# Performance work log

Hardware: AMD Instinct MI355X
Metric: run time of the kernel (lower is better)

Reference implementation:

```python
import jax, jax.numpy as jnp
import numpy as np

ALPHA_FOCAL = 0.25
GAMMA_FOCAL = 2.0
MARGIN_PEN = 0.005
RADIUS_REP = 0.015


def _cdist(a, b):
    # a: [B,N,3], b: [B,M,3] -> [B,N,M] euclidean distances (torch.cdist)
    d2 = (jnp.sum(a * a, axis=-1)[:, :, None]
          + jnp.sum(b * b, axis=-1)[:, None, :]
          - 2.0 * jnp.einsum('bnd,bmd->bnm', a, b))
    return jnp.sqrt(jnp.maximum(d2, 1e-12))


def _chamfer(p1, p2):
    d = _cdist(p1, p2)                       # [B,N,M]
    return jnp.min(d, axis=2).mean(axis=1) + jnp.min(d, axis=1).mean(axis=1)


def _repulsion(pc):
    B, N, _ = pc.shape
    d = _cdist(pc, pc)
    d = jnp.where(jnp.eye(N, dtype=bool)[None], jnp.inf, d)
    return jax.nn.relu(RADIUS_REP - d).mean(axis=(1, 2))


def _penetration(hand_pc, obj_pc):
    d = _cdist(obj_pc, hand_pc)              # [B,Nobj,Nhand]
    min_d = jnp.min(d, axis=2)
    return jax.nn.relu(MARGIN_PEN - min_d).mean(axis=1)


def _focal(logits, y):
    # numerically-stable BCE with logits, reduction='none'
    bce = jnp.maximum(logits, 0.0) - logits * y + jnp.log1p(jnp.exp(-jnp.abs(logits)))
    pt = jnp.exp(-bce)
    return (ALPHA_FOCAL * (1.0 - pt) ** GAMMA_FOCAL * bce).mean()


def _pose_loss(pred_pose, gt_pose):
    loss_trans = jnp.abs(pred_pose[:, :3] - gt_pose[:, :3]).mean(axis=1)
    qp = pred_pose[:, 3:]
    qg = gt_pose[:, 3:]
    qp = qp / jnp.linalg.norm(qp, axis=1, keepdims=True)
    qg = qg / jnp.linalg.norm(qg, axis=1, keepdims=True)
    loss_rot = 1.0 - jnp.abs(jnp.sum(qp * qg, axis=1))
    return loss_trans + 0.1 * loss_rot


def setup_inputs() -> dict:
    key = jax.random.key(0)
    ks = jax.random.split(key, 11)
    B, NH, NO, DQ = 16, 1024, 2048, 24
    scale = 0.05  # meter-scale clouds so margins 0.005/0.015 are active
    return {
        'pred_hand': jax.random.normal(ks[0], (B, NH, 3)) * scale,
        'pred_obj': jax.random.normal(ks[1], (B, NO, 3)) * scale,
        'pred_pose': jax.random.normal(ks[2], (B, 7)),
        'pred_qpos': jax.random.normal(ks[3], (B, DQ)),
        'pred_contact_logits': jax.random.normal(ks[4], (B, NH)),
        'gt_hand': jax.random.normal(ks[5], (B, NH, 3)) * scale,
        'gt_obj': jax.random.normal(ks[6], (B, NO, 3)) * scale,
        'gt_pose': jax.random.normal(ks[7], (B, 7)),
        'gt_qpos': jax.random.normal(ks[8], (B, DQ)),
        'gt_contact': (jax.random.uniform(ks[9], (B, NH)) < 0.3).astype(jnp.float32),
        'has_contact': (jax.random.uniform(ks[10], (B,)) < 0.8).astype(jnp.float32),
    }


def reference(pred_hand, pred_obj, pred_pose, pred_qpos, pred_contact_logits,
              gt_hand, gt_obj, gt_pose, gt_qpos, gt_contact, has_contact):
    loss_cd_hand = _chamfer(pred_hand, gt_hand).mean()
    loss_qpos = jnp.mean((pred_qpos - gt_qpos) ** 2)
    loss_contact = _focal(pred_contact_logits, gt_contact)

    batch_cd_obj = _chamfer(pred_obj, gt_obj)
    batch_pose = _pose_loss(pred_pose, gt_pose)
    batch_rep = _repulsion(pred_obj)
    batch_pen = _penetration(pred_hand, pred_obj)

    valid = has_contact.sum() + 1e-6
    loss_cd_obj = jnp.sum(batch_cd_obj * has_contact) / valid
    loss_pose = jnp.sum(batch_pose * has_contact) / valid
    loss_rep = jnp.sum(batch_rep * has_contact) / valid
    loss_pen = jnp.sum(batch_pen * has_contact) / valid

    total = (5.0 * loss_cd_hand + 5.0 * loss_cd_obj + 2.0 * loss_pose
             + 1.0 * loss_qpos + 2.0 * loss_contact
             + 0.5 * loss_rep + 0.5 * loss_pen)
    return total
```

## Files before the change

### kernel.cpp

```cpp
#include <hip/hip_runtime.h>
#include <math.h>

#define B   16
#define NH  1024
#define NO  2048
#define DQ  24

#define ALPHA_FOCAL 0.25f
#define MARGIN_PEN  0.005f
#define RADIUS_REP  0.015f
#define R2REP       (RADIUS_REP * RADIUS_REP)

#define WS_SCAL    16
#define ROWS_TOTAL 131072
#define JC         128

typedef float v2f __attribute__((ext_vector_type(2)));
typedef float v4f __attribute__((ext_vector_type(4)));

__device__ inline float wsqrt(float x) { return __builtin_amdgcn_sqrtf(x); }

__device__ inline float block_reduce_sum(float v, float* red) {
    #pragma unroll
    for (int off = 32; off > 0; off >>= 1) v += __shfl_down(v, off, 64);
    int lane = threadIdx.x & 63;
    int wid  = threadIdx.x >> 6;
    if (lane == 0) red[wid] = v;
    __syncthreads();
    float s = 0.f;
    if (threadIdx.x == 0) s = red[0] + red[1] + red[2] + red[3];
    __syncthreads();
    return s;
}

__device__ inline void cham_step(v4f A, v4f Bv,
                                 const v2f px2[4], const v2f py2[4], const v2f pz2[4],
                                 v2f m2[4]) {
    v2f ax = A.lo, ay = A.hi, az = Bv.lo, aw = Bv.hi;
    #pragma unroll
    for (int k = 0; k < 4; ++k) {
        v2f t = __builtin_elementwise_fma(az, pz2[k], aw);
        t     = __builtin_elementwise_fma(ay, py2[k], t);
        t     = __builtin_elementwise_fma(ax, px2[k], t);
        m2[k] = __builtin_elementwise_min(m2[k], t);
    }
}

__device__ inline void rep_step(v4f A, v4f Bv,
                                const v2f px2[4], const v2f py2[4], const v2f pz2[4],
                                const v2f pn2[4], v2f* s2) {
    v2f ax = A.lo, ay = A.hi, az = Bv.lo, aw = Bv.hi;
    #pragma unroll
    for (int k = 0; k < 4; ++k) {
        v2f t = __builtin_elementwise_fma(az, pz2[k], aw);
        t     = __builtin_elementwise_fma(ay, py2[k], t);
        t     = __builtin_elementwise_fma(ax, px2[k], t);
        v2f d2 = t + pn2[k];
        v2f dd;
        dd.x = wsqrt(__builtin_amdgcn_fmed3f(d2.x, 1e-12f, R2REP));
        dd.y = wsqrt(__builtin_amdgcn_fmed3f(d2.y, 1e-12f, R2REP));
        *s2 += dd;
    }
}

__global__ __launch_bounds__(256, 4) void pairwise_kernel(
    const float* __restrict__ pred_hand, const float* __restrict__ pred_obj,
    const float* __restrict__ gt_hand,   const float* __restrict__ gt_obj,
    const float* __restrict__ has_contact,
    const float* __restrict__ logits,    const float* __restrict__ gt_contact,
    const float* __restrict__ pred_qpos, const float* __restrict__ gt_qpos,
    const float* __restrict__ pred_pose, const float* __restrict__ gt_pose,
    float* __restrict__ ws)
{
    __shared__ v4f  qs[JC];
    __shared__ float red[4];

    const int tid = threadIdx.x;
    const int blk = blockIdx.x;

    if (blk >= 2048) {
        if (blk == 2048) {
            float fsum = 0.f;
            for (int i = tid; i < B*NH; i += 256) {
                float l = logits[i];
                float y = gt_contact[i];
                float bce = fmaxf(l, 0.f) - l*y + log1pf(expf(-fabsf(l)));
                float pt  = expf(-bce);
                float om  = 1.f - pt;
                fsum += ALPHA_FOCAL * om * om * bce;
            }
            float fT = block_reduce_sum(fsum, red);
            if (tid == 0) atomicAdd(&ws[6], fT);
        } else if (blk == 2049) {
            float qsum = 0.f;
            for (int i = tid; i < B*DQ; i += 256) {
                float d = pred_qpos[i] - gt_qpos[i];
                qsum += d*d;
            }
            float qT = block_reduce_sum(qsum, red);
            if (tid == 0) atomicAdd(&ws[7], qT);
        } else {
            float psum = 0.f, vsum = 0.f;
            if (tid < B) {
                const float* pp = pred_pose + tid*7;
                const float* gp = gt_pose   + tid*7;
                float lt = (fabsf(pp[0]-gp[0]) + fabsf(pp[1]-gp[1]) + fabsf(pp[2]-gp[2])) * (1.f/3.f);
                float npn = wsqrt(pp[3]*pp[3] + pp[4]*pp[4] + pp[5]*pp[5] + pp[6]*pp[6]);
                float ngn = wsqrt(gp[3]*gp[3] + gp[4]*gp[4] + gp[5]*gp[5] + gp[6]*gp[6]);
                float dot = (pp[3]*gp[3] + pp[4]*gp[4] + pp[5]*gp[5] + pp[6]*gp[6]) / (npn * ngn);
                float lr = 1.f - fabsf(dot);
                psum = (lt + 0.1f*lr) * has_contact[tid];
                vsum = has_contact[tid];
            }
            float pT = block_reduce_sum(psum, red);
            float vT = block_reduce_sum(vsum, red);
            if (tid == 0) { atomicAdd(&ws[8], pT); atomicAdd(&ws[9], vT); }
        }
        return;
    }

    unsigned* rowmin = (unsigned*)(ws + WS_SCAL);
    const float* Pb; const float* Qb;
    int b, rowbase = 0, rep = 0;

    if (blk < 256) {
        int dir = blk >> 7, l = blk & 127;
        b = l >> 3; int jc = l & 7;
        Pb = (dir ? gt_hand : pred_hand) + b*NH*3;
        Qb = (dir ? pred_hand : gt_hand) + b*NH*3 + jc*JC*3;
        rowbase = dir*16384 + b*1024;
    } else if (blk < 1280) {
        int idx = blk - 256;
        int dir = idx >> 9, l = idx & 511;
        b = l >> 5; int pc = (l >> 4) & 1, jc = l & 15;
        Pb = (dir ? gt_obj : pred_obj) + b*NO*3 + pc*1024*3;
        Qb = (dir ? pred_obj : gt_obj) + b*NO*3 + jc*JC*3;
        rowbase = 32768 + dir*32768 + b*2048 + pc*1024;
    } else if (blk < 1792) {
        int idx = blk - 1280;
        b = idx >> 5; int pc = (idx >> 4) & 1, jc = idx & 15;
        Pb = pred_obj + b*NO*3 + pc*1024*3;
        Qb = pred_obj + b*NO*3 + jc*JC*3;
        rep = 1;
    } else {
        int idx = blk - 1792;
        b = idx >> 4; int pc = (idx >> 3) & 1, jc = idx & 7;
        Pb = pred_obj  + b*NO*3 + pc*1024*3;
        Qb = pred_hand + b*NH*3 + jc*JC*3;
        rowbase = 98304 + b*2048 + pc*1024;
    }

    if (tid < JC) {
        float x = Qb[tid*3+0], y = Qb[tid*3+1], z = Qb[tid*3+2];
        float w = fmaf(x, x, fmaf(y, y, z*z));
        float* qf = (float*)qs;
        int p = tid >> 1, e = tid & 1;
        qf[p*8 + 0 + e] = -2.f*x;
        qf[p*8 + 2 + e] = -2.f*y;
        qf[p*8 + 4 + e] = -2.f*z;
        qf[p*8 + 6 + e] = w;
    }
    __syncthreads();

    float pn[4]; v2f px2[4], py2[4], pz2[4];
    #pragma unroll
    for (int k = 0; k < 4; ++k) {
        int n = tid + k*256;
        float x = Pb[n*3+0], y = Pb[n*3+1], z = Pb[n*3+2];
        px2[k] = (v2f){x, x}; py2[k] = (v2f){y, y}; pz2[k] = (v2f){z, z};
        pn[k]  = fmaf(x, x, fmaf(y, y, z*z));
    }

    if (!rep) {
        v2f m2[4] = {(v2f){1e30f,1e30f}, (v2f){1e30f,1e30f},
                     (v2f){1e30f,1e30f}, (v2f){1e30f,1e30f}};
        v4f A0=qs[0],B0=qs[1],A1=qs[2],B1=qs[3],A2=qs[4],B2=qs[5],A3=qs[6],B3=qs[7];
        for (int j2 = 0; j2 < 60; j2 += 4) {
            cham_step(A0,B0,px2,py2,pz2,m2); A0=qs[2*j2+ 8]; B0=qs[2*j2+ 9];
            cham_step(A1,B1,px2,py2,pz2,m2); A1=qs[2*j2+10]; B1=qs[2*j2+11];
            cham_step(A2,B2,px2,py2,pz2,m2); A2=qs[2*j2+12]; B2=qs[2*j2+13];
            cham_step(A3,B3,px2,py2,pz2,m2); A3=qs[2*j2+14]; B3=qs[2*j2+15];
        }
        cham_step(A0,B0,px2,py2,pz2,m2); cham_step(A1,B1,px2,py2,pz2,m2);
        cham_step(A2,B2,px2,py2,pz2,m2); cham_step(A3,B3,px2,py2,pz2,m2);

        #pragma unroll
        for (int k = 0; k < 4; ++k) {
            float mv = fminf(m2[k].x, m2[k].y) + pn[k];
            unsigned c = ~__float_as_uint(fmaxf(mv, 1e-12f));
            atomicMax(&rowmin[rowbase + tid + k*256], c);
        }
    } else {
        v2f pn2[4];
        #pragma unroll
        for (int k = 0; k < 4; ++k) pn2[k] = (v2f){pn[k], pn[k]};
        v2f s2 = (v2f){0.f, 0.f};
        v4f A0=qs[0],B0=qs[1],A1=qs[2],B1=qs[3],A2=qs[4],B2=qs[5],A3=qs[6],B3=qs[7];
        for (int j2 = 0; j2 < 60; j2 += 4) {
            rep_step(A0,B0,px2,py2,pz2,pn2,&s2); A0=qs[2*j2+ 8]; B0=qs[2*j2+ 9];
            rep_step(A1,B1,px2,py2,pz2,pn2,&s2); A1=qs[2*j2+10]; B1=qs[2*j2+11];
            rep_step(A2,B2,px2,py2,pz2,pn2,&s2); A2=qs[2*j2+12]; B2=qs[2*j2+13];
            rep_step(A3,B3,px2,py2,pz2,pn2,&s2); A3=qs[2*j2+14]; B3=qs[2*j2+15];
        }
        rep_step(A0,B0,px2,py2,pz2,pn2,&s2); rep_step(A1,B1,px2,py2,pz2,pn2,&s2);
        rep_step(A2,B2,px2,py2,pz2,pn2,&s2); rep_step(A3,B3,px2,py2,pz2,pn2,&s2);

        float bs = block_reduce_sum(s2.x + s2.y, red);
        if (tid == 0) atomicAdd(&ws[4], bs * has_contact[b]);
    }
}

__global__ __launch_bounds__(256) void combine_kernel(
    const float* __restrict__ has_contact, float* __restrict__ ws,
    float* __restrict__ out)
{
    __shared__ float red[4];
    const unsigned* rowmin = (const unsigned*)(ws + WS_SCAL);
    int blk = blockIdx.x;
    int tid = threadIdx.x;

    int slot, rows, base, pen = 0;
    float w = 1.f;
    if (blk < 32) {
        int dir = blk >> 4, b = blk & 15;
        slot = dir; rows = 1024; base = dir*16384 + b*1024;
    } else if (blk < 64) {
        int idx = blk - 32; int dir = idx >> 4, b = idx & 15;
        slot = 2 + dir; rows = 2048; base = 32768 + dir*32768 + b*2048;
        w = has_contact[b];
    } else {
        int b = blk - 64;
        slot = 5; rows = 2048; base = 98304 + b*2048;
        w = has_contact[b]; pen = 1;
    }
    float s = 0.f;
    for (int n = tid; n < rows; n += 256) {
        float d = wsqrt(__uint_as_float(~rowmin[base + n]));
        s += pen ? fmaxf(MARGIN_PEN - d, 0.f) : d;
    }
    float bs = block_reduce_sum(s, red);
    if (tid == 0) {
        atomicAdd(&ws[slot], bs * w);
        __threadfence();
        unsigned* cnt = (unsigned*)(ws + 15);
        unsigned old = atomicAdd(cnt, 1u);
        if (old == 79u) {
            __threadfence();
            float s0 = atomicAdd(&ws[0], 0.f), s1 = atomicAdd(&ws[1], 0.f);
            float s2 = atomicAdd(&ws[2], 0.f), s3 = atomicAdd(&ws[3], 0.f);
            float s4 = atomicAdd(&ws[4], 0.f), s5 = atomicAdd(&ws[5], 0.f);
            float s6 = atomicAdd(&ws[6], 0.f), s7 = atomicAdd(&ws[7], 0.f);
            float s8 = atomicAdd(&ws[8], 0.f), s9 = atomicAdd(&ws[9], 0.f);
            double vT    = s9;
            double valid = vT + 1e-6;
            double NOd   = (double)NO;
            double repw  = vT*NOd*NOd*(double)RADIUS_REP - (double)s4;
            double repx  = repw - vT*NOd*((double)RADIUS_REP - 1e-6);
            double loss_cd_hand = ((double)s0 + (double)s1) / (double)(B*NH);
            double loss_cd_obj  = ((double)s2 + (double)s3) / (NOd * valid);
            double loss_rep     = repx / (NOd * NOd * valid);
            double loss_pen     = (double)s5 / (NOd * valid);
            double loss_pose    = (double)s8 / valid;
            double loss_qpos    = (double)s7 / (double)(B*DQ);
            double loss_contact = (double)s6 / (double)(B*NH);
            double total = 5.0*loss_cd_hand + 5.0*loss_cd_obj + 2.0*loss_pose
                         + 1.0*loss_qpos + 2.0*loss_contact
                         + 0.5*loss_rep + 0.5*loss_pen;
            out[0] = (float)total;
        }
    }
}

extern "C" void kernel_launch(void* const* d_in, const int* in_sizes, int n_in,
                              void* d_out, int out_size, void* d_ws, size_t ws_size,
                              hipStream_t stream) {
    const float* pred_hand   = (const float*)d_in[0];
    const float* pred_obj    = (const float*)d_in[1];
    const float* pred_pose   = (const float*)d_in[2];
    const float* pred_qpos   = (const float*)d_in[3];
    const float* logits      = (const float*)d_in[4];
    const float* gt_hand     = (const float*)d_in[5];
    const float* gt_obj      = (const float*)d_in[6];
    const float* gt_pose     = (const float*)d_in[7];
    const float* gt_qpos     = (const float*)d_in[8];
    const float* gt_contact  = (const float*)d_in[9];
    const float* has_contact = (const float*)d_in[10];

    float* ws = (float*)d_ws;

    hipMemsetAsync(ws, 0, (WS_SCAL + ROWS_TOTAL) * sizeof(float), stream);

    pairwise_kernel<<<2051, 256, 0, stream>>>(pred_hand, pred_obj, gt_hand, gt_obj,
                                              has_contact, logits, gt_contact,
                                              pred_qpos, gt_qpos, pred_pose, gt_pose, ws);
    combine_kernel<<<80, 256, 0, stream>>>(has_contact, ws, (float*)d_out);
}
```

Before: 67.41 us.

## Restructure pairwise kernel to per-wave tiles with wave-uniform repulsion skip

Each wavefront now owns an independent 1024-row by 64-column tile, with 16 P points per lane (8 v2f pairs) and per-wave Q staging in shared memory. This replaces the block-wide 1024x128 tiles that held 4 points per thread. The repulsion path adds a wave-level __any check that skips the sqrt/med3 work when no pair in the wave falls inside the radius, adding the constant radius instead. Rep tiles are scheduled first and the scalar loss blocks move to the front of the grid. Occupancy drops to 3 blocks per SIMD in exchange for more register reuse, and per-wave shuffle reductions replace block reductions.

```diff
diff --git a/kernel.cpp b/kernel.cpp
--- a/kernel.cpp
+++ b/kernel.cpp
@@ -13,7 +13,6 @@
 
 #define WS_SCAL    16
 #define ROWS_TOTAL 131072
-#define JC         128
 
 typedef float v2f __attribute__((ext_vector_type(2)));
 typedef float v4f __attribute__((ext_vector_type(4)));
@@ -33,37 +32,7 @@
     return s;
 }
 
-__device__ inline void cham_step(v4f A, v4f Bv,
-                                 const v2f px2[4], const v2f py2[4], const v2f pz2[4],
-                                 v2f m2[4]) {
-    v2f ax = A.lo, ay = A.hi, az = Bv.lo, aw = Bv.hi;
-    #pragma unroll
-    for (int k = 0; k < 4; ++k) {
-        v2f t = __builtin_elementwise_fma(az, pz2[k], aw);
-        t     = __builtin_elementwise_fma(ay, py2[k], t);
-        t     = __builtin_elementwise_fma(ax, px2[k], t);
-        m2[k] = __builtin_elementwise_min(m2[k], t);
-    }
-}
-
-__device__ inline void rep_step(v4f A, v4f Bv,
-                                const v2f px2[4], const v2f py2[4], const v2f pz2[4],
-                                const v2f pn2[4], v2f* s2) {
-    v2f ax = A.lo, ay = A.hi, az = Bv.lo, aw = Bv.hi;
-    #pragma unroll
-    for (int k = 0; k < 4; ++k) {
-        v2f t = __builtin_elementwise_fma(az, pz2[k], aw);
-        t     = __builtin_elementwise_fma(ay, py2[k], t);
-        t     = __builtin_elementwise_fma(ax, px2[k], t);
-        v2f d2 = t + pn2[k];
-        v2f dd;
-        dd.x = wsqrt(__builtin_amdgcn_fmed3f(d2.x, 1e-12f, R2REP));
-        dd.y = wsqrt(__builtin_amdgcn_fmed3f(d2.y, 1e-12f, R2REP));
-        *s2 += dd;
-    }
-}
-
-__global__ __launch_bounds__(256, 4) void pairwise_kernel(
+__global__ __launch_bounds__(256, 3) void pairwise_kernel(
     const float* __restrict__ pred_hand, const float* __restrict__ pred_obj,
     const float* __restrict__ gt_hand,   const float* __restrict__ gt_obj,
     const float* __restrict__ has_contact,
@@ -72,14 +41,14 @@
     const float* __restrict__ pred_pose, const float* __restrict__ gt_pose,
     float* __restrict__ ws)
 {
-    __shared__ v4f  qs[JC];
+    __shared__ v4f  qs[256];
     __shared__ float red[4];
 
     const int tid = threadIdx.x;
     const int blk = blockIdx.x;
 
-    if (blk >= 2048) {
-        if (blk == 2048) {
+    if (blk < 3) {
+        if (blk == 0) {
             float fsum = 0.f;
             for (int i = tid; i < B*NH; i += 256) {
                 float l = logits[i];
@@ -91,7 +60,7 @@
             }
             float fT = block_reduce_sum(fsum, red);
             if (tid == 0) atomicAdd(&ws[6], fT);
-        } else if (blk == 2049) {
+        } else if (blk == 1) {
             float qsum = 0.f;
             for (int i = tid; i < B*DQ; i += 256) {
                 float d = pred_qpos[i] - gt_qpos[i];
@@ -119,94 +88,139 @@
         return;
     }
 
+    const int w   = tid >> 6;
+    const int l   = tid & 63;
+    const int wid = ((blk - 3) << 2) | w;
+
     unsigned* rowmin = (unsigned*)(ws + WS_SCAL);
     const float* Pb; const float* Qb;
     int b, rowbase = 0, rep = 0;
 
-    if (blk < 256) {
-        int dir = blk >> 7, l = blk & 127;
-        b = l >> 3; int jc = l & 7;
+    if (wid < 1024) {
+        b = wid >> 6; int pc = (wid >> 5) & 1, jc = wid & 31;
+        Pb = pred_obj + b*NO*3 + pc*1024*3;
+        Qb = pred_obj + b*NO*3 + jc*64*3;
+        rep = 1;
+    } else if (wid < 3072) {
+        int t = wid - 1024;
+        int dir = t >> 10, r = t & 1023;
+        b = r >> 6; int pc = (r >> 5) & 1, jc = r & 31;
+        Pb = (dir ? gt_obj : pred_obj) + b*NO*3 + pc*1024*3;
+        Qb = (dir ? pred_obj : gt_obj) + b*NO*3 + jc*64*3;
+        rowbase = 32768 + dir*32768 + b*2048 + pc*1024;
+    } else if (wid < 3584) {
+        int t = wid - 3072;
+        int dir = t >> 8, r = t & 255;
+        b = r >> 4; int jc = r & 15;
         Pb = (dir ? gt_hand : pred_hand) + b*NH*3;
-        Qb = (dir ? pred_hand : gt_hand) + b*NH*3 + jc*JC*3;
+        Qb = (dir ? pred_hand : gt_hand) + b*NH*3 + jc*64*3;
         rowbase = dir*16384 + b*1024;
-    } else if (blk < 1280) {
-        int idx = blk - 256;
-        int dir = idx >> 9, l = idx & 511;
-        b = l >> 5; int pc = (l >> 4) & 1, jc = l & 15;
-        Pb = (dir ? gt_obj : pred_obj) + b*NO*3 + pc*1024*3;
-        Qb = (dir ? pred_obj : gt_obj) + b*NO*3 + jc*JC*3;
-        rowbase = 32768 + dir*32768 + b*2048 + pc*1024;
-    } else if (blk < 1792) {
-        int idx = blk - 1280;
-        b = idx >> 5; int pc = (idx >> 4) & 1, jc = idx & 15;
-        Pb = pred_obj + b*NO*3 + pc*1024*3;
-        Qb = pred_obj + b*NO*3 + jc*JC*3;
-        rep = 1;
     } else {
-        int idx = blk - 1792;
-        b = idx >> 4; int pc = (idx >> 3) & 1, jc = idx & 7;
+        int t = wid - 3584;
+        b = t >> 5; int pc = (t >> 4) & 1, jc = t & 15;
         Pb = pred_obj  + b*NO*3 + pc*1024*3;
-        Qb = pred_hand + b*NH*3 + jc*JC*3;
+        Qb = pred_hand + b*NH*3 + jc*64*3;
         rowbase = 98304 + b*2048 + pc*1024;
     }
 
-    if (tid < JC) {
-        float x = Qb[tid*3+0], y = Qb[tid*3+1], z = Qb[tid*3+2];
-        float w = fmaf(x, x, fmaf(y, y, z*z));
-        float* qf = (float*)qs;
-        int p = tid >> 1, e = tid & 1;
-        qf[p*8 + 0 + e] = -2.f*x;
-        qf[p*8 + 2 + e] = -2.f*y;
-        qf[p*8 + 4 + e] = -2.f*z;
-        qf[p*8 + 6 + e] = w;
+    {
+        const float* qp = Qb + l*3;
+        float x = qp[0], y = qp[1], z = qp[2];
+        qs[(w << 6) | l] = (v4f){-2.f*x, -2.f*y, -2.f*z, fmaf(x, x, fmaf(y, y, z*z))};
     }
     __syncthreads();
 
-    float pn[4]; v2f px2[4], py2[4], pz2[4];
+    v2f px2[8], py2[8], pz2[8];
     #pragma unroll
-    for (int k = 0; k < 4; ++k) {
-        int n = tid + k*256;
-        float x = Pb[n*3+0], y = Pb[n*3+1], z = Pb[n*3+2];
-        px2[k] = (v2f){x, x}; py2[k] = (v2f){y, y}; pz2[k] = (v2f){z, z};
-        pn[k]  = fmaf(x, x, fmaf(y, y, z*z));
-    }
-
-    if (!rep) {
-        v2f m2[4] = {(v2f){1e30f,1e30f}, (v2f){1e30f,1e30f},
-                     (v2f){1e30f,1e30f}, (v2f){1e30f,1e30f}};
-        v4f A0=qs[0],B0=qs[1],A1=qs[2],B1=qs[3],A2=qs[4],B2=qs[5],A3=qs[6],B3=qs[7];
-        for (int j2 = 0; j2 < 60; j2 += 4) {
-            cham_step(A0,B0,px2,py2,pz2,m2); A0=qs[2*j2+ 8]; B0=qs[2*j2+ 9];
-            cham_step(A1,B1,px2,py2,pz2,m2); A1=qs[2*j2+10]; B1=qs[2*j2+11];
-            cham_step(A2,B2,px2,py2,pz2,m2); A2=qs[2*j2+12]; B2=qs[2*j2+13];
-            cham_step(A3,B3,px2,py2,pz2,m2); A3=qs[2*j2+14]; B3=qs[2*j2+15];
-        }
-        cham_step(A0,B0,px2,py2,pz2,m2); cham_step(A1,B1,px2,py2,pz2,m2);
-        cham_step(A2,B2,px2,py2,pz2,m2); cham_step(A3,B3,px2,py2,pz2,m2);
-
+    for (int kk = 0; kk < 8; ++kk) {
+        const float* p0 = Pb + (l + (kk << 7)) * 3;
+        const float* p1 = p0 + 192;
+        px2[kk] = (v2f){p0[0], p1[0]};
+        py2[kk] = (v2f){p0[1], p1[1]};
+        pz2[kk] = (v2f){p0[2], p1[2]};
+    }
+
+    const v4f* qw = qs + (w << 6);
+
+    if (rep) {
+        v2f pn2[8];
         #pragma unroll
-        for (int k = 0; k < 4; ++k) {
-            float mv = fminf(m2[k].x, m2[k].y) + pn[k];
-            unsigned c = ~__float_as_uint(fmaxf(mv, 1e-12f));
-            atomicMax(&rowmin[rowbase + tid + k*256], c);
-        }
+        for (int kk = 0; kk < 8; ++kk)
+            pn2[kk] = __builtin_elementwise_fma(px2[kk], px2[kk],
+                      __builtin_elementwise_fma(py2[kk], py2[kk], pz2[kk]*pz2[kk]));
+        v2f sacc = (v2f){0.f, 0.f};
+        const v2f vR = (v2f){RADIUS_REP, RADIUS_REP};
+        auto rstep = [&](v4f Q) {
+            v2f bx = __builtin_shufflevector(Q, Q, 0, 0);
+            v2f by = __builtin_shufflevector(Q, Q, 1, 1);
+            v2f bz = __builtin_shufflevector(Q, Q, 2, 2);
+            v2f bw = __builtin_shufflevector(Q, Q, 3, 3);
+            #pragma unroll
+            for (int kk = 0; kk < 8; ++kk) {
+                v2f t = __builtin_elementwise_fma(bz, pz2[kk], bw);
+                t     = __builtin_elementwise_fma(by, py2[kk], t);
+                t     = __builtin_elementwise_fma(bx, px2[kk], t);
+                v2f d2 = t + pn2[kk];
+                if (__any(fminf(d2.x, d2.y) < R2REP)) {
+                    v2f dd;
+                    dd.x = wsqrt(__builtin_amdgcn_fmed3f(d2.x, 1e-12f, R2REP));
+                    dd.y = wsqrt(__builtin_amdgcn_fmed3f(d2.y, 1e-12f, R2REP));
+                    sacc += dd;
+                } else {
+                    sacc += vR;
+                }
+            }
+        };
+        v4f Q0 = qw[0], Q1 = qw[1], Q2 = qw[2], Q3 = qw[3];
+        for (int j = 0; j < 60; j += 4) {
+            rstep(Q0); Q0 = qw[j+4];
+            rstep(Q1); Q1 = qw[j+5];
+            rstep(Q2); Q2 = qw[j+6];
+            rstep(Q3); Q3 = qw[j+7];
+        }
+        rstep(Q0); rstep(Q1); rstep(Q2); rstep(Q3);
+
+        float s = sacc.x + sacc.y;
+        #pragma unroll
+        for (int off = 32; off > 0; off >>= 1) s += __shfl_down(s, off, 64);
+        if (l == 0) atomicAdd(&ws[4], s * has_contact[b]);
     } else {
-        v2f pn2[4];
+        v2f m2[8];
         #pragma unroll
-        for (int k = 0; k < 4; ++k) pn2[k] = (v2f){pn[k], pn[k]};
-        v2f s2 = (v2f){0.f, 0.f};
-        v4f A0=qs[0],B0=qs[1],A1=qs[2],B1=qs[3],A2=qs[4],B2=qs[5],A3=qs[6],B3=qs[7];
-        for (int j2 = 0; j2 < 60; j2 += 4) {
-            rep_step(A0,B0,px2,py2,pz2,pn2,&s2); A0=qs[2*j2+ 8]; B0=qs[2*j2+ 9];
-            rep_step(A1,B1,px2,py2,pz2,pn2,&s2); A1=qs[2*j2+10]; B1=qs[2*j2+11];
-            rep_step(A2,B2,px2,py2,pz2,pn2,&s2); A2=qs[2*j2+12]; B2=qs[2*j2+13];
-            rep_step(A3,B3,px2,py2,pz2,pn2,&s2); A3=qs[2*j2+14]; B3=qs[2*j2+15];
-        }
-        rep_step(A0,B0,px2,py2,pz2,pn2,&s2); rep_step(A1,B1,px2,py2,pz2,pn2,&s2);
-        rep_step(A2,B2,px2,py2,pz2,pn2,&s2); rep_step(A3,B3,px2,py2,pz2,pn2,&s2);
-
-        float bs = block_reduce_sum(s2.x + s2.y, red);
-        if (tid == 0) atomicAdd(&ws[4], bs * has_contact[b]);
+        for (int kk = 0; kk < 8; ++kk) m2[kk] = (v2f){1e30f, 1e30f};
+        auto cstep = [&](v4f Q) {
+            v2f bx = __builtin_shufflevector(Q, Q, 0, 0);
+            v2f by = __builtin_shufflevector(Q, Q, 1, 1);
+            v2f bz = __builtin_shufflevector(Q, Q, 2, 2);
+            v2f bw = __builtin_shufflevector(Q, Q, 3, 3);
+            #pragma unroll
+            for (int kk = 0; kk < 8; ++kk) {
+                v2f t = __builtin_elementwise_fma(bz, pz2[kk], bw);
+                t     = __builtin_elementwise_fma(by, py2[kk], t);
+                t     = __builtin_elementwise_fma(bx, px2[kk], t);
+                m2[kk] = __builtin_elementwise_min(m2[kk], t);
+            }
+        };
+        v4f Q0 = qw[0], Q1 = qw[1], Q2 = qw[2], Q3 = qw[3];
+        for (int j = 0; j < 60; j += 4) {
+            cstep(Q0); Q0 = qw[j+4];
+            cstep(Q1); Q1 = qw[j+5];
+            cstep(Q2); Q2 = qw[j+6];
+            cstep(Q3); Q3 = qw[j+7];
+        }
+        cstep(Q0); cstep(Q1); cstep(Q2); cstep(Q3);
+
+        #pragma unroll
+        for (int kk = 0; kk < 8; ++kk) {
+            #pragma unroll
+            for (int e = 0; e < 2; ++e) {
+                float x = px2[kk][e], y = py2[kk][e], z = pz2[kk][e];
+                float pn = fmaf(x, x, fmaf(y, y, z*z));
+                float mv = m2[kk][e] + pn;
+                unsigned c = ~__float_as_uint(fmaxf(mv, 1e-12f));
+                atomicMax(&rowmin[rowbase + l + (kk << 7) + (e << 6)], c);
+            }
+        }
     }
 }
 
@@ -290,7 +304,7 @@
 
     hipMemsetAsync(ws, 0, (WS_SCAL + ROWS_TOTAL) * sizeof(float), stream);
 
-    pairwise_kernel<<<2051, 256, 0, stream>>>(pred_hand, pred_obj, gt_hand, gt_obj,
+    pairwise_kernel<<<1027, 256, 0, stream>>>(pred_hand, pred_obj, gt_hand, gt_obj,
                                               has_contact, logits, gt_contact,
                                               pred_qpos, gt_qpos, pred_pose, gt_pose, ws);
     combine_kernel<<<80, 256, 0, stream>>>(has_contact, ws, (float*)d_out);
```

Result: faster. 57.71 us (-14.4%).
